# Kernel tuning notes

Measured on AMD Instinct MI355X. Metric: run time of the kernel, lower is better.

## Reference

```python
import jax, jax.numpy as jnp
import numpy as np

FEATURES = 8
POINTS = 3
CLASSES = 128
BATCH = 1024
TEMPERATURE = 0.1


def setup_inputs() -> dict:
    key = jax.random.key(0)
    k1, k2, k3 = jax.random.split(key, 3)
    x = jax.random.normal(k1, (BATCH, FEATURES), dtype=jnp.float32)
    beta = jax.random.uniform(k2, (FEATURES, POINTS), dtype=jnp.float32)
    classifier = jax.random.uniform(
        k3, ((POINTS + 1) ** FEATURES, CLASSES), dtype=jnp.float32)
    return {"x": x, "beta": beta, "classifier": classifier}


def reference(x, beta, classifier):
    # b: sort beta ascending per-feature, negate, cumsum, prepend a zero bin edge
    T = 1.0 / TEMPERATURE
    bneg = jnp.cumsum(-jnp.sort(beta, axis=1), axis=1)            # [F, P]
    b = jnp.concatenate(
        [jnp.zeros((beta.shape[0], 1), beta.dtype), bneg], axis=1)  # [F, P+1]
    w = jnp.arange(1, POINTS + 2, dtype=x.dtype)                  # [P+1]
    # soft one-hot binning per feature: [B, F, P+1]
    logits = (x[:, :, None] * w[None, None, :] + b[None, :, :]) * T
    hot = jax.nn.softmax(logits, axis=-1)
    # iterative outer product over features -> joint leaf histogram [B, (P+1)^F]
    B = x.shape[0]
    leaves = hot[:, 0, :]
    for f in range(1, FEATURES):  # small fixed loop over features
        leaves = (leaves[:, :, None] * hot[:, f, None, :]).reshape(B, -1)
    return leaves @ classifier  # [B, classes]
```

## Files before the change

kernel.cpp:

```cpp
#include <hip/hip_runtime.h>
#include <stdint.h>

typedef unsigned short u16;
typedef __attribute__((ext_vector_type(4))) float f32x4;
typedef __attribute__((ext_vector_type(2))) float f32x2;
typedef __attribute__((ext_vector_type(8))) short s16x8;

#define T_INV 10.0f

__device__ __forceinline__ u16 f2bf(float f) {
  uint32_t u = __float_as_uint(f);
  uint32_t r = (u + 0x7FFFu + ((u >> 16) & 1u)) >> 16;
  return (u16)r;
}

__device__ __forceinline__ void gload_lds16(const void* g, void* l) {
  __builtin_amdgcn_global_load_lds(
      (const __attribute__((address_space(1))) uint32_t*)(g),
      (__attribute__((address_space(3))) uint32_t*)(l),
      16, 0, 0);
}

__global__ __launch_bounds__(256) void k_prep(
    const float* __restrict__ cls, const float* __restrict__ x,
    const float* __restrict__ beta,
    u16* __restrict__ ct, u16* __restrict__ plo, float* __restrict__ phiT)
{
  const int t = threadIdx.x;
  if (blockIdx.x < 1024) {
    __shared__ float tile[64 * 132];
    const int k0 = blockIdx.x * 64;
#pragma unroll
    for (int it = 0; it < 8; ++it) {
      int e = it * 1024 + t * 4;
      int r = e >> 7;
      int c = e & 127;
      f32x4 v = *(const f32x4*)(cls + (size_t)(k0 + r) * 128 + c);
      *(f32x4*)(tile + r * 132 + c) = v;
    }
    __syncthreads();
    const int c  = t >> 1;
    const int kh = t & 1;
    u16 vals[32];
#pragma unroll
    for (int j = 0; j < 32; ++j)
      vals[j] = f2bf(tile[(kh*32 + j) * 132 + c]);
    u16* dst = ct + ((size_t)(k0 >> 3) + kh * 4) * 1024 + c * 8;
#pragma unroll
    for (int qq = 0; qq < 4; ++qq) {
      s16x8 v;
#pragma unroll
      for (int e2 = 0; e2 < 8; ++e2) v[e2] = (short)vals[qq*8 + e2];
      *(s16x8*)(dst + (size_t)qq * 1024) = v;
    }
  } else {
    const int b = (blockIdx.x - 1024) * 64 + (t >> 2);
    const int q = t & 3;
    float hot[8][4];
#pragma unroll
    for (int f = 0; f < 8; ++f) {
      float b0 = beta[f*3+0], b1 = beta[f*3+1], b2 = beta[f*3+2];
      float s0 = fminf(b0, fminf(b1, b2));
      float s2 = fmaxf(b0, fmaxf(b1, b2));
      float s1 = b0 + b1 + b2 - s0 - s2;
      float bv1 = -s0, bv2 = -(s0 + s1), bv3 = -(s0 + s1 + s2);
      float xf = x[b*8 + f];
      float l0 = (xf * 1.0f       ) * T_INV;
      float l1 = (xf * 2.0f + bv1) * T_INV;
      float l2 = (xf * 3.0f + bv2) * T_INV;
      float l3 = (xf * 4.0f + bv3) * T_INV;
      float mm = fmaxf(fmaxf(l0, l1), fmaxf(l2, l3));
      float e0 = __expf(l0 - mm), e1 = __expf(l1 - mm);
      float e2 = __expf(l2 - mm), e3 = __expf(l3 - mm);
      float inv = 1.0f / (e0 + e1 + e2 + e3);
      hot[f][0] = e0*inv; hot[f][1] = e1*inv; hot[f][2] = e2*inv; hot[f][3] = e3*inv;
    }
    {
      float h23[16];
#pragma unroll
      for (int i2 = 0; i2 < 4; ++i2)
#pragma unroll
        for (int i3 = 0; i3 < 4; ++i3) h23[i2*4+i3] = hot[2][i2] * hot[3][i3];
      float h0q = hot[0][q];
#pragma unroll
      for (int i1 = 0; i1 < 4; ++i1) {
        float c01 = h0q * hot[1][i1];
#pragma unroll
        for (int j = 0; j < 16; ++j)
          phiT[(size_t)(q*64 + i1*16 + j) * 1024 + b] = c01 * h23[j];
      }
    }
    {
      float h67[16];
#pragma unroll
      for (int i6 = 0; i6 < 4; ++i6)
#pragma unroll
        for (int i7 = 0; i7 < 4; ++i7) h67[i6*4+i7] = hot[6][i6] * hot[7][i7];
      float h4q = hot[4][q];
      u16* dst = plo + (size_t)b*256 + q*64;
#pragma unroll
      for (int i5 = 0; i5 < 4; ++i5) {
        float c45 = h4q * hot[5][i5];
#pragma unroll
        for (int j = 0; j < 16; j += 8) {
          s16x8 v;
#pragma unroll
          for (int e = 0; e < 8; ++e) v[e] = (short)f2bf(c45 * h67[j+e]);
          *(s16x8*)(dst + i5*16 + j) = v;
        }
      }
    }
  }
}

__global__ __launch_bounds__(256, 2) void k_main(
    const u16* __restrict__ plo, const float* __restrict__ phiT,
    const u16* __restrict__ ct, u16* __restrict__ pws)
{
  __shared__ __align__(16) u16 As[32768];
  __shared__ __align__(16) u16 Bb[2][4096];

  const int wg  = blockIdx.x;
  const int xcd = wg & 7;
  const int idx = wg >> 3;
  const int hig = xcd * 8 + (idx >> 3);
  const int m   = idx & 7;

  const int t    = threadIdx.x;
  const int l    = t & 63;
  const int w    = t >> 6;
  const int lrow = l & 15;
  const int kg   = l >> 4;
  const int rbase = (w & 1) * 64;
  const int cbase = (w >> 1) * 64;

  const u16* ploM = plo + (size_t)m * 128 * 256;

#pragma unroll
  for (int i = 0; i < 16; ++i) {
    int ks  = i >> 1;
    int row = (i & 1) * 64 + (t >> 2);
    int g   = ((t & 3) - ((t >> 3) & 3)) & 3;
    gload_lds16(ploM + (size_t)row * 256 + ks * 32 + g * 8, &As[i * 2048 + t * 8]);
  }

  const int bc = t & 127;
  const int bg = t >> 7;
  const u16* bsrc = ct + (size_t)hig * 128 * 1024 + (size_t)bc * 8
                       + (size_t)bg * 1024;
  const int s0 = (bg + ((bc >> 1) & 3)) & 3;
  const int s2 = ((bg + 2) + ((bc >> 1) & 3)) & 3;

  s16x8 bregE0, bregE1, bregO0, bregO1;
  bregE0 = *(const s16x8*)(bsrc + 0 * 4096);
  bregE1 = *(const s16x8*)(bsrc + 0 * 4096 + 2048);
  bregO0 = *(const s16x8*)(bsrc + 1 * 4096);
  bregO1 = *(const s16x8*)(bsrc + 1 * 4096 + 2048);
  *(s16x8*)(&Bb[0][bc * 32 + s0 * 8]) = bregE0;
  *(s16x8*)(&Bb[0][bc * 32 + s2 * 8]) = bregE1;
  __syncthreads();

  f32x4 acc[4][4], hacc[4][4];
#pragma unroll
  for (int i = 0; i < 4; ++i)
#pragma unroll
    for (int j = 0; j < 4; ++j) { acc[i][j] = (f32x4)0.0f; hacc[i][j] = (f32x4)0.0f; }

#pragma unroll 1
  for (int h = 0; h < 4; ++h) {
#pragma unroll
    for (int ks = 0; ks < 8; ++ks) {
      const int tt = h * 8 + ks;
      if (h < 3 || ks < 6) {
        const u16* p = bsrc + (size_t)(tt + 2) * 4096;
        if (ks & 1) { bregO0 = *(const s16x8*)p; bregO1 = *(const s16x8*)(p + 2048); }
        else        { bregE0 = *(const s16x8*)p; bregE1 = *(const s16x8*)(p + 2048); }
      }
      s16x8 afr[4], bfr[4];
      const u16* Ak = &As[ks * 4096];
#pragma unroll
      for (int mt = 0; mt < 4; ++mt) {
        int row = rbase + mt * 16 + lrow;
        int s = (kg + ((row >> 1) & 3)) & 3;
        afr[mt] = *(const s16x8*)(Ak + row * 32 + s * 8);
      }
#pragma unroll
      for (int nt = 0; nt < 4; ++nt) {
        int c = cbase + nt * 16 + lrow;
        int s = (kg + ((c >> 1) & 3)) & 3;
        bfr[nt] = *(const s16x8*)(&Bb[ks & 1][c * 32 + s * 8]);
      }
#pragma unroll
      for (int mt = 0; mt < 4; ++mt)
#pragma unroll
        for (int nt = 0; nt < 4; ++nt)
          hacc[mt][nt] = __builtin_amdgcn_mfma_f32_16x16x32_bf16(
              afr[mt], bfr[nt], hacc[mt][nt], 0, 0, 0);
      if (h < 3 || ks < 7) {
        u16* d = &Bb[(ks + 1) & 1][bc * 32];
        if (ks & 1) { *(s16x8*)(d + s0 * 8) = bregE0; *(s16x8*)(d + s2 * 8) = bregE1; }
        else        { *(s16x8*)(d + s0 * 8) = bregO0; *(s16x8*)(d + s2 * 8) = bregO1; }
      }
      asm volatile("s_waitcnt lgkmcnt(0)" ::: "memory");
      __builtin_amdgcn_sched_barrier(0);
      __builtin_amdgcn_s_barrier();
      __builtin_amdgcn_sched_barrier(0);
    }
#pragma unroll
    for (int mt = 0; mt < 4; ++mt) {
      f32x4 p4 = *(const f32x4*)(phiT + (size_t)(hig * 4 + h) * 1024
                                 + m * 128 + rbase + mt * 16 + kg * 4);
#pragma unroll
      for (int r = 0; r < 4; ++r)
#pragma unroll
        for (int nt = 0; nt < 4; ++nt)
          acc[mt][nt][r] += p4[r] * hacc[mt][nt][r];
#pragma unroll
      for (int nt = 0; nt < 4; ++nt) hacc[mt][nt] = (f32x4)0.0f;
    }
  }

  __syncthreads();
  {
    u16* ob = As;
#pragma unroll
    for (int mt = 0; mt < 4; ++mt)
#pragma unroll
      for (int r = 0; r < 4; ++r) {
        int row = rbase + mt * 16 + kg * 4 + r;
#pragma unroll
        for (int nt = 0; nt < 4; ++nt) {
          int col = cbase + nt * 16 + lrow;
          ob[row * 136 + col] = f2bf(acc[mt][nt][r]);
        }
      }
    __syncthreads();
    const int row  = t >> 1;
    const int half = t & 1;
    const u16* srcp = ob + row * 136 + half * 64;
    u16* gdst = pws + ((size_t)hig * 1024 + (size_t)m * 128) * 128
                    + row * 128 + half * 64;
#pragma unroll
    for (int i = 0; i < 8; ++i)
      *(s16x8*)(gdst + i * 8) = *(const s16x8*)(srcp + i * 8);
  }
}

__global__ __launch_bounds__(256) void k_reduce(
    const u16* __restrict__ p, float* __restrict__ out)
{
  const int g = blockIdx.x * 256 + threadIdx.x;
  const u16* src = p + (size_t)g * 2;
  float a0 = 0.0f, a1 = 0.0f;
#pragma unroll 8
  for (int hig = 0; hig < 64; ++hig) {
    uint32_t v = *(const uint32_t*)(src + (size_t)hig * 131072);
    a0 += __uint_as_float((v & 0xFFFFu) << 16);
    a1 += __uint_as_float(v & 0xFFFF0000u);
  }
  f32x2 o; o.x = a0; o.y = a1;
  *(f32x2*)(out + (size_t)g * 2) = o;
}

extern "C" void kernel_launch(void* const* d_in, const int* in_sizes, int n_in,
                              void* d_out, int out_size, void* d_ws, size_t ws_size,
                              hipStream_t stream)
{
  const float* x    = (const float*)d_in[0];
  const float* beta = (const float*)d_in[1];
  const float* cls  = (const float*)d_in[2];
  float* out = (float*)d_out;

  char* ws = (char*)d_ws;
  u16*   ct   = (u16*)ws;
  u16*   plo  = (u16*)(ws + (16u << 20));
  float* phiT = (float*)(ws + (16u << 20) + 524288);
  u16*   pws  = (u16*)(ws + (16u << 20) + 524288 + 1048576);

  k_prep<<<1040, 256, 0, stream>>>(cls, x, beta, ct, plo, phiT);
  k_main<<<512, 256, 0, stream>>>(plo, phiT, ct, pws);
  k_reduce<<<256, 256, 0, stream>>>(pws, out);
}
```

Baseline: 45.48 us.

## Load B fragments directly from global into registers, drop LDS staging and barriers

Removes the double-buffered LDS staging of the classifier (B) tiles. Each lane now loads its MFMA B fragments straight from global memory into registers, using an even/odd register double buffer. This removes the per-k-step LDS writes, LDS reads and workgroup barriers. In exchange, each wave reads B independently, so global/L2 traffic is duplicated across the two row-waves, and the loads are exposed to latency with only one step of prefetch.

```diff
diff --git a/kernel.cpp b/kernel.cpp
--- a/kernel.cpp
+++ b/kernel.cpp
@@ -118,7 +118,6 @@
     const u16* __restrict__ ct, u16* __restrict__ pws)
 {
   __shared__ __align__(16) u16 As[32768];
-  __shared__ __align__(16) u16 Bb[2][4096];
 
   const int wg  = blockIdx.x;
   const int xcd = wg & 7;
@@ -143,68 +142,75 @@
     int g   = ((t & 3) - ((t >> 3) & 3)) & 3;
     gload_lds16(ploM + (size_t)row * 256 + ks * 32 + g * 8, &As[i * 2048 + t * 8]);
   }
-
-  const int bc = t & 127;
-  const int bg = t >> 7;
-  const u16* bsrc = ct + (size_t)hig * 128 * 1024 + (size_t)bc * 8
-                       + (size_t)bg * 1024;
-  const int s0 = (bg + ((bc >> 1) & 3)) & 3;
-  const int s2 = ((bg + 2) + ((bc >> 1) & 3)) & 3;
-
-  s16x8 bregE0, bregE1, bregO0, bregO1;
-  bregE0 = *(const s16x8*)(bsrc + 0 * 4096);
-  bregE1 = *(const s16x8*)(bsrc + 0 * 4096 + 2048);
-  bregO0 = *(const s16x8*)(bsrc + 1 * 4096);
-  bregO1 = *(const s16x8*)(bsrc + 1 * 4096 + 2048);
-  *(s16x8*)(&Bb[0][bc * 32 + s0 * 8]) = bregE0;
-  *(s16x8*)(&Bb[0][bc * 32 + s2 * 8]) = bregE1;
-  __syncthreads();
+  __builtin_amdgcn_sched_barrier(0);
+  asm volatile("s_waitcnt vmcnt(0)" ::: "memory");
+  __builtin_amdgcn_sched_barrier(0);
+  __builtin_amdgcn_s_barrier();
+  __builtin_amdgcn_sched_barrier(0);
+
+  const u16* bW = ct + (size_t)hig * 131072 + (size_t)kg * 1024
+                     + (size_t)(cbase + lrow) * 8;
 
   f32x4 acc[4][4], hacc[4][4];
 #pragma unroll
   for (int i = 0; i < 4; ++i)
 #pragma unroll
     for (int j = 0; j < 4; ++j) { acc[i][j] = (f32x4)0.0f; hacc[i][j] = (f32x4)0.0f; }
+
+  s16x8 bE[4], bO[4];
+#pragma unroll
+  for (int nt = 0; nt < 4; ++nt) bE[nt] = *(const s16x8*)(bW + nt * 128);
 
 #pragma unroll 1
   for (int h = 0; h < 4; ++h) {
-#pragma unroll
-    for (int ks = 0; ks < 8; ++ks) {
-      const int tt = h * 8 + ks;
-      if (h < 3 || ks < 6) {
-        const u16* p = bsrc + (size_t)(tt + 2) * 4096;
-        if (ks & 1) { bregO0 = *(const s16x8*)p; bregO1 = *(const s16x8*)(p + 2048); }
-        else        { bregE0 = *(const s16x8*)p; bregE1 = *(const s16x8*)(p + 2048); }
-      }
-      s16x8 afr[4], bfr[4];
-      const u16* Ak = &As[ks * 4096];
-#pragma unroll
-      for (int mt = 0; mt < 4; ++mt) {
-        int row = rbase + mt * 16 + lrow;
-        int s = (kg + ((row >> 1) & 3)) & 3;
-        afr[mt] = *(const s16x8*)(Ak + row * 32 + s * 8);
-      }
-#pragma unroll
-      for (int nt = 0; nt < 4; ++nt) {
-        int c = cbase + nt * 16 + lrow;
-        int s = (kg + ((c >> 1) & 3)) & 3;
-        bfr[nt] = *(const s16x8*)(&Bb[ks & 1][c * 32 + s * 8]);
-      }
-#pragma unroll
-      for (int mt = 0; mt < 4; ++mt)
+    const u16* bh = bW + (size_t)h * 32768;
+#pragma unroll
+    for (int ks2 = 0; ks2 < 4; ++ks2) {
+      const int ksA = ks2 * 2, ksB = ksA + 1;
+#pragma unroll
+      for (int nt = 0; nt < 4; ++nt)
+        bO[nt] = *(const s16x8*)(bh + ksB * 4096 + nt * 128);
+      {
+        s16x8 afr[4];
+        const u16* Ak = &As[ksA * 4096];
+#pragma unroll
+        for (int mt = 0; mt < 4; ++mt) {
+          int row = rbase + mt * 16 + lrow;
+          int s = (kg + ((row >> 1) & 3)) & 3;
+          afr[mt] = *(const s16x8*)(Ak + row * 32 + s * 8);
+        }
+#pragma unroll
+        for (int mt = 0; mt < 4; ++mt)
+#pragma unroll
+          for (int nt = 0; nt < 4; ++nt)
+            hacc[mt][nt] = __builtin_amdgcn_mfma_f32_16x16x32_bf16(
+                afr[mt], bE[nt], hacc[mt][nt], 0, 0, 0);
+      }
+      if (ks2 < 3) {
 #pragma unroll
         for (int nt = 0; nt < 4; ++nt)
-          hacc[mt][nt] = __builtin_amdgcn_mfma_f32_16x16x32_bf16(
-              afr[mt], bfr[nt], hacc[mt][nt], 0, 0, 0);
-      if (h < 3 || ks < 7) {
-        u16* d = &Bb[(ks + 1) & 1][bc * 32];
-        if (ks & 1) { *(s16x8*)(d + s0 * 8) = bregE0; *(s16x8*)(d + s2 * 8) = bregE1; }
-        else        { *(s16x8*)(d + s0 * 8) = bregO0; *(s16x8*)(d + s2 * 8) = bregO1; }
-      }
-      asm volatile("s_waitcnt lgkmcnt(0)" ::: "memory");
-      __builtin_amdgcn_sched_barrier(0);
-      __builtin_amdgcn_s_barrier();
-      __builtin_amdgcn_sched_barrier(0);
+          bE[nt] = *(const s16x8*)(bh + (ksA + 2) * 4096 + nt * 128);
+      } else if (h < 3) {
+#pragma unroll
+        for (int nt = 0; nt < 4; ++nt)
+          bE[nt] = *(const s16x8*)(bh + 32768 + nt * 128);
+      }
+      {
+        s16x8 afr[4];
+        const u16* Ak = &As[ksB * 4096];
+#pragma unroll
+        for (int mt = 0; mt < 4; ++mt) {
+          int row = rbase + mt * 16 + lrow;
+          int s = (kg + ((row >> 1) & 3)) & 3;
+          afr[mt] = *(const s16x8*)(Ak + row * 32 + s * 8);
+        }
+#pragma unroll
+        for (int mt = 0; mt < 4; ++mt)
+#pragma unroll
+          for (int nt = 0; nt < 4; ++nt)
+            hacc[mt][nt] = __builtin_amdgcn_mfma_f32_16x16x32_bf16(
+                afr[mt], bO[nt], hacc[mt][nt], 0, 0, 0);
+      }
     }
 #pragma unroll
     for (int mt = 0; mt < 4; ++mt) {
```

Measured after the change: 56.55 us. 1.24x slower.

## Fold per-chunk phi scaling into running accumulator via ratio rescaling

Applied to the files above, without the earlier changes.

The separate hacc accumulator is replaced by rescaling a single accumulator with the ratio of consecutive phi values (clamped by an epsilon), plus a final multiply by the last phi. This frees 64 accumulator registers and removes the per-chunk fused add. The A-fragment LDS reads are software-prefetched one k-step ahead with precomputed offsets, and MFMA issue is wrapped in s_setprio. The ratio trick adds rounding and clamping error when phi values are tiny, so accuracy could drift from the original.

```diff
diff --git a/kernel.cpp b/kernel.cpp
--- a/kernel.cpp
+++ b/kernel.cpp
@@ -7,6 +7,7 @@
 typedef __attribute__((ext_vector_type(8))) short s16x8;
 
 #define T_INV 10.0f
+#define QEPS 9.5367431640625e-07f
 
 __device__ __forceinline__ u16 f2bf(float f) {
   uint32_t u = __float_as_uint(f);
@@ -144,9 +145,21 @@
     gload_lds16(ploM + (size_t)row * 256 + ks * 32 + g * 8, &As[i * 2048 + t * 8]);
   }
 
+  int aoff[4], boff[4];
+#pragma unroll
+  for (int mt = 0; mt < 4; ++mt) {
+    int row = rbase + mt * 16 + lrow;
+    aoff[mt] = row * 32 + (((kg + ((row >> 1) & 3)) & 3)) * 8;
+  }
+#pragma unroll
+  for (int nt = 0; nt < 4; ++nt) {
+    int c = cbase + nt * 16 + lrow;
+    boff[nt] = c * 32 + (((kg + ((c >> 1) & 3)) & 3)) * 8;
+  }
+
   const int bc = t & 127;
   const int bg = t >> 7;
-  const u16* bsrc = ct + (size_t)hig * 128 * 1024 + (size_t)bc * 8
+  const u16* bsrc = ct + (size_t)hig * 131072 + (size_t)bc * 8
                        + (size_t)bg * 1024;
   const int s0 = (bg + ((bc >> 1) & 3)) & 3;
   const int s2 = ((bg + 2) + ((bc >> 1) & 3)) & 3;
@@ -160,11 +173,27 @@
   *(s16x8*)(&Bb[0][bc * 32 + s2 * 8]) = bregE1;
   __syncthreads();
 
-  f32x4 acc[4][4], hacc[4][4];
+  f32x4 qprev[4];
+  {
+    const float* p0 = phiT + (size_t)(hig * 4) * 1024 + m * 128;
+#pragma unroll
+    for (int mt = 0; mt < 4; ++mt) {
+      f32x4 q = *(const f32x4*)(p0 + rbase + mt * 16 + kg * 4);
+#pragma unroll
+      for (int r = 0; r < 4; ++r) qprev[mt][r] = fmaxf(q[r], QEPS);
+    }
+  }
+
+  f32x4 acc[4][4];
 #pragma unroll
   for (int i = 0; i < 4; ++i)
 #pragma unroll
-    for (int j = 0; j < 4; ++j) { acc[i][j] = (f32x4)0.0f; hacc[i][j] = (f32x4)0.0f; }
+    for (int j = 0; j < 4; ++j) acc[i][j] = (f32x4)0.0f;
+
+  s16x8 afrP[4];
+#pragma unroll
+  for (int mt = 0; mt < 4; ++mt)
+    afrP[mt] = *(const s16x8*)(&As[aoff[mt]]);
 
 #pragma unroll 1
   for (int h = 0; h < 4; ++h) {
@@ -176,26 +205,24 @@
         if (ks & 1) { bregO0 = *(const s16x8*)p; bregO1 = *(const s16x8*)(p + 2048); }
         else        { bregE0 = *(const s16x8*)p; bregE1 = *(const s16x8*)(p + 2048); }
       }
-      s16x8 afr[4], bfr[4];
-      const u16* Ak = &As[ks * 4096];
-#pragma unroll
-      for (int mt = 0; mt < 4; ++mt) {
-        int row = rbase + mt * 16 + lrow;
-        int s = (kg + ((row >> 1) & 3)) & 3;
-        afr[mt] = *(const s16x8*)(Ak + row * 32 + s * 8);
-      }
-#pragma unroll
-      for (int nt = 0; nt < 4; ++nt) {
-        int c = cbase + nt * 16 + lrow;
-        int s = (kg + ((c >> 1) & 3)) & 3;
-        bfr[nt] = *(const s16x8*)(&Bb[ks & 1][c * 32 + s * 8]);
-      }
+      s16x8 bfr[4];
+#pragma unroll
+      for (int nt = 0; nt < 4; ++nt)
+        bfr[nt] = *(const s16x8*)(&Bb[ks & 1][boff[nt]]);
+      __builtin_amdgcn_s_setprio(1);
 #pragma unroll
       for (int mt = 0; mt < 4; ++mt)
 #pragma unroll
         for (int nt = 0; nt < 4; ++nt)
-          hacc[mt][nt] = __builtin_amdgcn_mfma_f32_16x16x32_bf16(
-              afr[mt], bfr[nt], hacc[mt][nt], 0, 0, 0);
+          acc[mt][nt] = __builtin_amdgcn_mfma_f32_16x16x32_bf16(
+              afrP[mt], bfr[nt], acc[mt][nt], 0, 0, 0);
+      __builtin_amdgcn_s_setprio(0);
+      {
+        const int nks = (ks + 1) & 7;
+#pragma unroll
+        for (int mt = 0; mt < 4; ++mt)
+          afrP[mt] = *(const s16x8*)(&As[nks * 4096 + aoff[mt]]);
+      }
       if (h < 3 || ks < 7) {
         u16* d = &Bb[(ks + 1) & 1][bc * 32];
         if (ks & 1) { *(s16x8*)(d + s0 * 8) = bregE0; *(s16x8*)(d + s2 * 8) = bregE1; }
@@ -206,17 +233,24 @@
       __builtin_amdgcn_s_barrier();
       __builtin_amdgcn_sched_barrier(0);
     }
-#pragma unroll
-    for (int mt = 0; mt < 4; ++mt) {
-      f32x4 p4 = *(const f32x4*)(phiT + (size_t)(hig * 4 + h) * 1024
-                                 + m * 128 + rbase + mt * 16 + kg * 4);
-#pragma unroll
-      for (int r = 0; r < 4; ++r)
+    if (h < 3) {
+      const float* pn = phiT + (size_t)(hig * 4 + h + 1) * 1024 + m * 128;
+#pragma unroll
+      for (int mt = 0; mt < 4; ++mt) {
+        f32x4 qn = *(const f32x4*)(pn + rbase + mt * 16 + kg * 4);
+        f32x4 ratio;
+#pragma unroll
+        for (int r = 0; r < 4; ++r) {
+          float q = fmaxf(qn[r], QEPS);
+          ratio[r] = qprev[mt][r] * __builtin_amdgcn_rcpf(q);
+          qprev[mt][r] = q;
+        }
 #pragma unroll
         for (int nt = 0; nt < 4; ++nt)
-          acc[mt][nt][r] += p4[r] * hacc[mt][nt][r];
-#pragma unroll
-      for (int nt = 0; nt < 4; ++nt) hacc[mt][nt] = (f32x4)0.0f;
+#pragma unroll
+          for (int r = 0; r < 4; ++r)
+            acc[mt][nt][r] *= ratio[r];
+      }
     }
   }
 
@@ -231,7 +265,7 @@
 #pragma unroll
         for (int nt = 0; nt < 4; ++nt) {
           int col = cbase + nt * 16 + lrow;
-          ob[row * 136 + col] = f2bf(acc[mt][nt][r]);
+          ob[row * 136 + col] = f2bf(acc[mt][nt][r] * qprev[mt][r]);
         }
       }
     __syncthreads();
```

After: 45.79 us. No clear change (+0.7%).
